# Performance work log

Hardware: AMD Instinct MI355X
Metric: run time of the kernel (lower is better)

The kernel has to match this reference:

```python
import jax, jax.numpy as jnp
import numpy as np

NEG_SLOPE = 0.2  # DGL GATConv default leaky_relu slope

N_NODES, N_EDGES = 50000, 800000
IN_FEATS, HID, OUT_FEATS, HEADS = 256, 64, 64, 3


def gat_conv(x, W, attn_l, attn_r, bias, src, dst, n_nodes, activation=True):
    """DGL-style GATConv. x:[N,F_in], W:[F_in,H*D], attn_l/attn_r/bias:[H,D]."""
    H, D = attn_l.shape
    feat = (x @ W).reshape(n_nodes, H, D)              # [N,H,D]
    el = jnp.sum(feat * attn_l, axis=-1)               # [N,H]
    er = jnp.sum(feat * attn_r, axis=-1)               # [N,H]
    e = jax.nn.leaky_relu(el[src] + er[dst], NEG_SLOPE)  # [E,H]
    # edge softmax over incoming edges of each dst node
    m = jax.ops.segment_max(e, dst, num_segments=n_nodes)  # [N,H] (-inf for isolated)
    ex = jnp.exp(e - m[dst])                            # [E,H]
    s = jax.ops.segment_sum(ex, dst, num_segments=n_nodes)  # [N,H]
    alpha = ex / s[dst]                                 # [E,H]
    msg = feat[src] * alpha[:, :, None]                 # [E,H,D]  (memory-bound gather)
    out = jax.ops.segment_sum(msg, dst, num_segments=n_nodes)  # [N,H,D]
    out = out + bias[None, :, :]
    return jax.nn.relu(out) if activation else out


def setup_inputs() -> dict:
    key = jax.random.key(0)
    ks = jax.random.split(key, 16)
    HD = HEADS * HID
    def glorot(k, shape):
        fan = sum(shape)
        return jax.random.normal(k, shape, jnp.float32) * jnp.sqrt(2.0 / fan)
    return {
        "features": jax.random.normal(ks[0], (N_NODES, IN_FEATS), jnp.float32),
        "src": jax.random.randint(ks[1], (N_EDGES,), 0, N_NODES, jnp.int32),
        "dst": jax.random.randint(ks[2], (N_EDGES,), 0, N_NODES, jnp.int32),
        "W1": glorot(ks[3], (IN_FEATS, HD)),
        "al1": glorot(ks[4], (HEADS, HID)),
        "ar1": glorot(ks[5], (HEADS, HID)),
        "b1": jnp.zeros((HEADS, HID), jnp.float32),
        "W2": glorot(ks[6], (HD, HD)),
        "al2": glorot(ks[7], (HEADS, HID)),
        "ar2": glorot(ks[8], (HEADS, HID)),
        "b2": jnp.zeros((HEADS, HID), jnp.float32),
        "Wm1": glorot(ks[9], (HD, HID)),
        "bm1": jnp.zeros((HID,), jnp.float32),
        "Wm2": glorot(ks[10], (HID, OUT_FEATS)),
        "bm2": jnp.zeros((OUT_FEATS,), jnp.float32),
    }


def reference(features, src, dst, W1, al1, ar1, b1, W2, al2, ar2, b2, Wm1, bm1, Wm2, bm2):
    n = features.shape[0]
    x = gat_conv(features, W1, al1, ar1, b1, src, dst, n).reshape(n, -1)  # [N, H*D]
    x = gat_conv(x, W2, al2, ar2, b2, src, dst, n).reshape(n, -1)        # [N, H*D]
    x = jax.nn.relu(x @ Wm1 + bm1)
    return x @ Wm2 + bm2                                                 # [N, out_feats]
```

## Files before the change

kernel.cpp:

```cpp
#include <hip/hip_runtime.h>
#include <hip/hip_bf16.h>

#define NN 50000
#define NE 800000
#define FIN 256
#define HEADS_H 3
#define HDIM 192
#define NEG_SLOPE 0.2f
#define CHUNK 128
#define SCAN_ELEMS 512
#define SCAN_NB ((NN + SCAN_ELEMS - 1) / SCAN_ELEMS)
#define BK 64
#define W1_PAD 200
#define W2_PAD 72
#define H_PAD 72

typedef __attribute__((ext_vector_type(8))) short frag8;
typedef __attribute__((ext_vector_type(4))) float f32x4;
typedef __attribute__((ext_vector_type(2))) unsigned u32x2;
typedef unsigned short u16;

__device__ inline u16 f2b(float x) {
    __hip_bfloat16 h = __float2bfloat16(x);
    return __builtin_bit_cast(u16, h);
}
__device__ inline float b2f(u16 b) {
    __hip_bfloat16 h = __builtin_bit_cast(__hip_bfloat16, b);
    return __bfloat162float(h);
}
__device__ inline float b2f_lo(unsigned v) { return __builtin_bit_cast(float, v << 16); }
__device__ inline float b2f_hi(unsigned v) { return __builtin_bit_cast(float, v & 0xffff0000u); }

__device__ inline int wave_sum_i(int v) {
#pragma unroll
    for (int off = 32; off > 0; off >>= 1) v += __shfl_xor(v, off, 64);
    return v;
}

__global__ void k_fill_pattern(u16* __restrict__ p, int n, u16 v) {
    int i = blockIdx.x * blockDim.x + threadIdx.x;
    if (i < n) p[i] = v;
}
__global__ void k_zero(int* __restrict__ p, int n) {
    int i = blockIdx.x * blockDim.x + threadIdx.x;
    if (i < n) p[i] = 0;
}

__global__ void k_sniff(const unsigned* __restrict__ p, int* __restrict__ flag) {
    __shared__ int cnt_s;
    if (threadIdx.x == 0) cnt_s = 0;
    __syncthreads();
    int c = 0;
    for (int i = threadIdx.x; i < 4096; i += 256) {
        float v = __builtin_bit_cast(float, p[i]);
        float a = fabsf(v);
        if (a > 1e-4f && a < 100.f) c++;
    }
    atomicAdd(&cnt_s, c);
    __syncthreads();
    if (threadIdx.x == 0) *flag = (cnt_s > 2048) ? 1 : 0;
}

__global__ void k_cvt8(const void* i0, const void* i1, const void* i2, const void* i3,
                       const void* i4, const void* i5, const void* i6, const void* i7,
                       u16* o0, u16* o1, u16* o2, u16* o3, u16* o4, u16* o5, u16* o6, u16* o7,
                       const int* __restrict__ flag) {
    const void* ins[8] = {i0, i1, i2, i3, i4, i5, i6, i7};
    u16* outs[8] = {o0, o1, o2, o3, o4, o5, o6, o7};
    const int ns[8] = {HDIM, HDIM, HDIM, HDIM, HDIM, HDIM, 64, 64};
    int b = blockIdx.x;
    int n = ns[b];
    const void* in = ins[b];
    u16* out = outs[b];
    int f = *flag;
    for (int i = threadIdx.x; i < n; i += 256) {
        out[i] = f ? f2b(((const float*)in)[i]) : ((const u16*)in)[i];
    }
}

__global__ void k_transpose4(const void* __restrict__ B0, const void* __restrict__ B1,
                             const void* __restrict__ B2, const void* __restrict__ B3,
                             u16* __restrict__ T0, u16* __restrict__ T1, u16* __restrict__ T2,
                             u16* __restrict__ T3, const int* __restrict__ flag) {
    const int n0 = FIN * HDIM, n1 = HDIM * HDIM, n2 = HDIM * 64, n3 = 64 * 64;
    int gi = blockIdx.x * 256 + threadIdx.x;
    const void* B;
    u16* T;
    int K, N, i;
    if (gi < n0) { B = B0; T = T0; K = FIN; N = HDIM; i = gi; }
    else if (gi < n0 + n1) { B = B1; T = T1; K = HDIM; N = HDIM; i = gi - n0; }
    else if (gi < n0 + n1 + n2) { B = B2; T = T2; K = HDIM; N = 64; i = gi - n0 - n1; }
    else if (gi < n0 + n1 + n2 + n3) { B = B3; T = T3; K = 64; N = 64; i = gi - n0 - n1 - n2; }
    else return;
    int k = i / N, n = i - k * N;
    u16 v = (*flag) ? f2b(((const float*)B)[i]) : ((const u16*)B)[i];
    T[n * K + k] = v;
}

__global__ void k_count(const int* __restrict__ dst, int* __restrict__ cnt, int E) {
    int e = blockIdx.x * blockDim.x + threadIdx.x;
    if (e < E) atomicAdd(&cnt[dst[e]], 1);
}

__global__ void k_scan_partial(const int* __restrict__ cnt, int* __restrict__ partial) {
    int b = blockIdx.x, t = threadIdx.x;
    int i0 = b * SCAN_ELEMS + t * 2;
    int v = 0;
    if (i0 < NN) v += cnt[i0];
    if (i0 + 1 < NN) v += cnt[i0 + 1];
    v = wave_sum_i(v);
    __shared__ int wsum[4];
    if ((t & 63) == 0) wsum[t >> 6] = v;
    __syncthreads();
    if (t == 0) partial[b] = wsum[0] + wsum[1] + wsum[2] + wsum[3];
}

__global__ void k_scan_mid(const int* __restrict__ partial, int* __restrict__ offsets,
                           int* __restrict__ indptr) {
    __shared__ int s[SCAN_NB];
    int t = threadIdx.x;
    if (t < SCAN_NB) s[t] = partial[t];
    __syncthreads();
    for (int off = 1; off < SCAN_NB; off <<= 1) {
        int v = (t >= off && t < SCAN_NB) ? s[t - off] : 0;
        __syncthreads();
        if (t < SCAN_NB) s[t] += v;
        __syncthreads();
    }
    if (t < SCAN_NB) offsets[t] = (t == 0) ? 0 : s[t - 1];
    if (t == 0) indptr[NN] = s[SCAN_NB - 1];
}

__global__ void k_scan_final(int* __restrict__ cnt, const int* __restrict__ offsets,
                             int* __restrict__ indptr) {
    __shared__ int tsum[256];
    int b = blockIdx.x, t = threadIdx.x;
    int i0 = b * SCAN_ELEMS + t * 2;
    int c0 = (i0 < NN) ? cnt[i0] : 0;
    int c1 = (i0 + 1 < NN) ? cnt[i0 + 1] : 0;
    tsum[t] = c0 + c1;
    __syncthreads();
    for (int off = 1; off < 256; off <<= 1) {
        int v = (t >= off) ? tsum[t - off] : 0;
        __syncthreads();
        tsum[t] += v;
        __syncthreads();
    }
    int excl = offsets[b] + ((t == 0) ? 0 : tsum[t - 1]);
    if (i0 < NN) { indptr[i0] = excl; cnt[i0] = excl; }
    if (i0 + 1 < NN) { indptr[i0 + 1] = excl + c0; cnt[i0 + 1] = excl + c0; }
}

__global__ void k_fill(const int* __restrict__ dst, const int* __restrict__ srcv,
                       int* __restrict__ cursor, int* __restrict__ src_perm, int E) {
    int e = blockIdx.x * blockDim.x + threadIdx.x;
    if (e < E) {
        int p = atomicAdd(&cursor[dst[e]], 1);
        src_perm[p] = srcv[e];
    }
}

__global__ __launch_bounds__(256) void k_gemm_lds(
    const void* __restrict__ A, int a_dual, const u16* __restrict__ BT,
    void* __restrict__ C, const int* __restrict__ flag, int M, int K,
    float* __restrict__ elp, float* __restrict__ erp,
    const u16* __restrict__ al, const u16* __restrict__ ar) {
    __shared__ u16 sB[2][12 * 64 * 8 * 2];
    const int tid = threadIdx.x;
    const int lane = tid & 63;
    const int w = tid >> 6;
    const int c16 = lane & 15;
    const int quad = lane >> 4;
    const int m_base = blockIdx.x * 64 + w * 16;
    const int f = *flag;
    const bool a32 = a_dual && f;

    int m0 = m_base + c16;
    int arow = (m0 < M) ? m0 : (M - 1);

    f32x4 acc[12];
#pragma unroll
    for (int t = 0; t < 12; ++t) acc[t] = (f32x4)0.f;

    frag8 v[6];
    auto stageLoad = [&](int c) {
        int k0 = c * BK;
#pragma unroll
        for (int s = 0; s < 6; ++s) {
            int g = tid + s * 256;
            int n = g >> 3, k8 = g & 7;
            v[s] = *(const frag8*)(BT + (size_t)n * K + k0 + k8 * 8);
        }
    };
    auto stageWrite = [&](int buf) {
#pragma unroll
        for (int s = 0; s < 6; ++s) {
            int g = tid + s * 256;
            int n = g >> 3, k8 = g & 7;
            int t = n >> 4, cc = n & 15, kk = k8 >> 2, qq = k8 & 3;
            int gl = (kk * 12 + t) * 64 + qq * 16 + cc;
            *(frag8*)&sB[buf][gl * 8] = v[s];
        }
    };
    auto loadAc = [&](int k0, frag8* a) {
#pragma unroll
        for (int kk = 0; kk < 2; ++kk) {
            if (a32) {
                const float* ap = (const float*)A + (size_t)arow * K + k0 + kk * 32 + quad * 8;
                f32x4 f0 = *(const f32x4*)ap;
                f32x4 f1 = *(const f32x4*)(ap + 4);
                a[kk][0] = (short)f2b(f0[0]); a[kk][1] = (short)f2b(f0[1]);
                a[kk][2] = (short)f2b(f0[2]); a[kk][3] = (short)f2b(f0[3]);
                a[kk][4] = (short)f2b(f1[0]); a[kk][5] = (short)f2b(f1[1]);
                a[kk][6] = (short)f2b(f1[2]); a[kk][7] = (short)f2b(f1[3]);
            } else {
                a[kk] = *(const frag8*)((const u16*)A + (size_t)arow * K + k0 + kk * 32 + quad * 8);
            }
        }
    };

    const int nc = K / BK;
    stageLoad(0);
    stageWrite(0);
    __syncthreads();
    for (int c = 0; c < nc; ++c) {
        if (c + 1 < nc) stageLoad(c + 1);
        frag8 a[2];
        loadAc(c * BK, a);
        const int buf = c & 1;
#pragma unroll
        for (int kk = 0; kk < 2; ++kk) {
#pragma unroll
            for (int t = 0; t < 12; ++t) {
                frag8 b = *(const frag8*)&sB[buf][((kk * 12 + t) * 64 + lane) * 8];
                acc[t] = __builtin_amdgcn_mfma_f32_16x16x32_bf16(a[kk], b, acc[t], 0, 0, 0);
            }
        }
        if (c + 1 < nc) stageWrite((c + 1) & 1);
        __syncthreads();
    }

#pragma unroll
    for (int t = 0; t < 12; ++t) {
        int col = t * 16 + c16;
#pragma unroll
        for (int rr = 0; rr < 4; ++rr) {
            int m = m_base + quad * 4 + rr;
            if (m < M)
                ((__hip_bfloat16*)C)[(size_t)m * HDIM + col] = __float2bfloat16(acc[t][rr]);
        }
    }

    float alv[12], arv[12];
#pragma unroll
    for (int t = 0; t < 12; ++t) {
        alv[t] = b2f(al[t * 16 + c16]);
        arv[t] = b2f(ar[t * 16 + c16]);
    }
#pragma unroll
    for (int rr = 0; rr < 4; ++rr) {
        int m = m_base + quad * 4 + rr;
        float pl[HEADS_H] = {0.f, 0.f, 0.f};
        float pr[HEADS_H] = {0.f, 0.f, 0.f};
#pragma unroll
        for (int t = 0; t < 12; ++t) {
            int h = t >> 2;
            pl[h] += acc[t][rr] * alv[t];
            pr[h] += acc[t][rr] * arv[t];
        }
#pragma unroll
        for (int h = 0; h < HEADS_H; ++h) {
#pragma unroll
            for (int off = 1; off < 16; off <<= 1) {
                pl[h] += __shfl_xor(pl[h], off, 64);
                pr[h] += __shfl_xor(pr[h], off, 64);
            }
            if (c16 == 0 && m < M) {
                elp[m * HEADS_H + h] = pl[h];
                erp[m * HEADS_H + h] = pr[h];
            }
        }
    }
}

__global__ __launch_bounds__(256) void k_mlp(const u16* __restrict__ xbf,
                                             const u16* __restrict__ Wm1T,
                                             const u16* __restrict__ Wm2T,
                                             const u16* __restrict__ bm1,
                                             const u16* __restrict__ bm2, void* __restrict__ out,
                                             const int* __restrict__ flag, int M) {
    __shared__ u16 sW1[64 * W1_PAD];
    __shared__ u16 sW2[64 * W2_PAD];
    __shared__ u16 sH[64 * H_PAD];
    const int tid = threadIdx.x;
    const int lane = tid & 63, w = tid >> 6;
    const int c16 = lane & 15, quad = lane >> 4;
    const int m_base = blockIdx.x * 64 + w * 16;
    const bool c32 = *flag != 0;

#pragma unroll
    for (int s = 0; s < 6; ++s) {
        int g = tid + s * 256;
        int n = g / 24, k8 = g - n * 24;
        *(frag8*)&sW1[n * W1_PAD + k8 * 8] = *(const frag8*)(Wm1T + n * 192 + k8 * 8);
    }
#pragma unroll
    for (int s = 0; s < 2; ++s) {
        int g = tid + s * 256;
        int n = g >> 3, k8 = g & 7;
        *(frag8*)&sW2[n * W2_PAD + k8 * 8] = *(const frag8*)(Wm2T + n * 64 + k8 * 8);
    }
    int m0 = m_base + c16;
    int arow = (m0 < M) ? m0 : (M - 1);
    __syncthreads();

    f32x4 acc1[4];
#pragma unroll
    for (int t = 0; t < 4; ++t) acc1[t] = (f32x4)0.f;
    for (int k0 = 0; k0 < 192; k0 += 32) {
        frag8 a = *(const frag8*)(xbf + (size_t)arow * HDIM + k0 + quad * 8);
#pragma unroll
        for (int t = 0; t < 4; ++t) {
            frag8 b = *(const frag8*)&sW1[(t * 16 + c16) * W1_PAD + k0 + quad * 8];
            acc1[t] = __builtin_amdgcn_mfma_f32_16x16x32_bf16(a, b, acc1[t], 0, 0, 0);
        }
    }
#pragma unroll
    for (int t = 0; t < 4; ++t) {
        float bv = b2f(bm1[t * 16 + c16]);
#pragma unroll
        for (int rr = 0; rr < 4; ++rr) {
            float v = fmaxf(acc1[t][rr] + bv, 0.f);
            sH[(w * 16 + quad * 4 + rr) * H_PAD + t * 16 + c16] = f2b(v);
        }
    }
    __syncthreads();

    f32x4 acc2[4];
#pragma unroll
    for (int t = 0; t < 4; ++t) acc2[t] = (f32x4)0.f;
#pragma unroll
    for (int k0 = 0; k0 < 64; k0 += 32) {
        frag8 a = *(const frag8*)&sH[(w * 16 + c16) * H_PAD + k0 + quad * 8];
#pragma unroll
        for (int t = 0; t < 4; ++t) {
            frag8 b = *(const frag8*)&sW2[(t * 16 + c16) * W2_PAD + k0 + quad * 8];
            acc2[t] = __builtin_amdgcn_mfma_f32_16x16x32_bf16(a, b, acc2[t], 0, 0, 0);
        }
    }
#pragma unroll
    for (int t = 0; t < 4; ++t) {
        int col = t * 16 + c16;
        float bv = b2f(bm2[col]);
#pragma unroll
        for (int rr = 0; rr < 4; ++rr) {
            int m = m_base + quad * 4 + rr;
            if (m < M) {
                float v = acc2[t][rr] + bv;
                if (c32) ((float*)out)[(size_t)m * 64 + col] = v;
                else ((__hip_bfloat16*)out)[(size_t)m * 64 + col] = __float2bfloat16(v);
            }
        }
    }
}

__global__ __launch_bounds__(256) void k_agg_sm(
    const u16* __restrict__ feat, const float* __restrict__ el, const float* __restrict__ er,
    const int* __restrict__ src_perm, const int* __restrict__ indptr,
    const u16* __restrict__ bias, u16* __restrict__ outb, int n_nodes) {
    __shared__ int ssrc_s[4][CHUNK];
    __shared__ float salpha_s[4][CHUNK * HEADS_H];
    const int wave = threadIdx.x >> 6, lane = threadIdx.x & 63;
    const int n = blockIdx.x * 4 + wave;
    if (n >= n_nodes) return;
    int* ssrc = ssrc_s[wave];
    float* salpha = salpha_s[wave];
    const int beg = indptr[n];
    const int lenT = indptr[n + 1] - beg;
    const float er0 = er[n * 3 + 0], er1 = er[n * 3 + 1], er2 = er[n * 3 + 2];
    const int u = lane;
    const int h = u >> 4;
    const u16* fbase = feat + 4 * u;

    float m0 = -INFINITY, m1 = -INFINITY, m2 = -INFINITY;
    float s0 = 0.f, s1 = 0.f, s2 = 0.f;
    float a0 = 0.f, a1 = 0.f, a2 = 0.f, a3 = 0.f;

    for (int c0 = 0; c0 < lenT; c0 += CHUNK) {
        const int len = min(CHUNK, lenT - c0);
        float cm0 = -INFINITY, cm1 = -INFINITY, cm2 = -INFINITY;
        for (int j = lane; j < len; j += 64) {
            int s = src_perm[beg + c0 + j];
            ssrc[j] = s;
            const float* ep = el + (size_t)s * 3;
            float e0 = ep[0] + er0, e1 = ep[1] + er1, e2 = ep[2] + er2;
            e0 = (e0 > 0.f) ? e0 : NEG_SLOPE * e0;
            e1 = (e1 > 0.f) ? e1 : NEG_SLOPE * e1;
            e2 = (e2 > 0.f) ? e2 : NEG_SLOPE * e2;
            salpha[j * 3 + 0] = e0;
            salpha[j * 3 + 1] = e1;
            salpha[j * 3 + 2] = e2;
            cm0 = fmaxf(cm0, e0); cm1 = fmaxf(cm1, e1); cm2 = fmaxf(cm2, e2);
        }
#pragma unroll
        for (int off = 32; off > 0; off >>= 1) {
            cm0 = fmaxf(cm0, __shfl_xor(cm0, off, 64));
            cm1 = fmaxf(cm1, __shfl_xor(cm1, off, 64));
            cm2 = fmaxf(cm2, __shfl_xor(cm2, off, 64));
        }
        float n0 = fmaxf(m0, cm0), n1 = fmaxf(m1, cm1), n2 = fmaxf(m2, cm2);
        float r0 = __expf(m0 - n0), r1 = __expf(m1 - n1), r2 = __expf(m2 - n2);
        __threadfence_block();
        float cs0 = 0.f, cs1 = 0.f, cs2 = 0.f;
        for (int j = lane; j < len; j += 64) {
            float ex0 = __expf(salpha[j * 3 + 0] - n0);
            float ex1 = __expf(salpha[j * 3 + 1] - n1);
            float ex2 = __expf(salpha[j * 3 + 2] - n2);
            salpha[j * 3 + 0] = ex0;
            salpha[j * 3 + 1] = ex1;
            salpha[j * 3 + 2] = ex2;
            cs0 += ex0; cs1 += ex1; cs2 += ex2;
        }
#pragma unroll
        for (int off = 32; off > 0; off >>= 1) {
            cs0 += __shfl_xor(cs0, off, 64);
            cs1 += __shfl_xor(cs1, off, 64);
            cs2 += __shfl_xor(cs2, off, 64);
        }
        s0 = s0 * r0 + cs0; s1 = s1 * r1 + cs1; s2 = s2 * r2 + cs2;
        m0 = n0; m1 = n1; m2 = n2;
        __threadfence_block();
        if (u < 48) {
            float rh = (h == 0) ? r0 : ((h == 1) ? r1 : r2);
            a0 *= rh; a1 *= rh; a2 *= rh; a3 *= rh;
            for (int j0 = 0; j0 < len; j0 += 4) {
                int jb = min(j0 + 1, len - 1), jc = min(j0 + 2, len - 1), jd = min(j0 + 3, len - 1);
                int sa = ssrc[j0], sb = ssrc[jb], sc = ssrc[jc], sd = ssrc[jd];
                float wa = salpha[j0 * 3 + h];
                float wb = (j0 + 1 < len) ? salpha[jb * 3 + h] : 0.f;
                float wc = (j0 + 2 < len) ? salpha[jc * 3 + h] : 0.f;
                float wd = (j0 + 3 < len) ? salpha[jd * 3 + h] : 0.f;
                u32x2 va = *(const u32x2*)(fbase + (size_t)sa * HDIM);
                u32x2 vb = *(const u32x2*)(fbase + (size_t)sb * HDIM);
                u32x2 vc = *(const u32x2*)(fbase + (size_t)sc * HDIM);
                u32x2 vd = *(const u32x2*)(fbase + (size_t)sd * HDIM);
                a0 += wa * b2f_lo(va.x); a1 += wa * b2f_hi(va.x);
                a2 += wa * b2f_lo(va.y); a3 += wa * b2f_hi(va.y);
                a0 += wb * b2f_lo(vb.x); a1 += wb * b2f_hi(vb.x);
                a2 += wb * b2f_lo(vb.y); a3 += wb * b2f_hi(vb.y);
                a0 += wc * b2f_lo(vc.x); a1 += wc * b2f_hi(vc.x);
                a2 += wc * b2f_lo(vc.y); a3 += wc * b2f_hi(vc.y);
                a0 += wd * b2f_lo(vd.x); a1 += wd * b2f_hi(vd.x);
                a2 += wd * b2f_lo(vd.y); a3 += wd * b2f_hi(vd.y);
            }
        }
    }

    if (u < 48) {
        float shh = (h == 0) ? s0 : ((h == 1) ? s1 : s2);
        float inv = (shh > 0.f) ? 1.f / shh : 0.f;
        u32x2 bv = *(const u32x2*)(bias + 4 * u);
        float v0 = a0 * inv + b2f_lo(bv.x);
        float v1 = a1 * inv + b2f_hi(bv.x);
        float v2 = a2 * inv + b2f_lo(bv.y);
        float v3 = a3 * inv + b2f_hi(bv.y);
        v0 = fmaxf(v0, 0.f); v1 = fmaxf(v1, 0.f);
        v2 = fmaxf(v2, 0.f); v3 = fmaxf(v3, 0.f);
        u32x2 o;
        o.x = (unsigned)f2b(v0) | ((unsigned)f2b(v1) << 16);
        o.y = (unsigned)f2b(v2) | ((unsigned)f2b(v3) << 16);
        *(u32x2*)(outb + (size_t)n * HDIM + 4 * u) = o;
    }
}

extern "C" void kernel_launch(void* const* d_in, const int* in_sizes, int n_in,
                              void* d_out, int out_size, void* d_ws, size_t ws_size,
                              hipStream_t stream) {
    const void* features = d_in[0];
    const int* src = (const int*)d_in[1];
    const int* dst = (const int*)d_in[2];
    const void* W1 = d_in[3];
    const void* al1 = d_in[4];
    const void* ar1 = d_in[5];
    const void* b1 = d_in[6];
    const void* W2 = d_in[7];
    const void* al2 = d_in[8];
    const void* ar2 = d_in[9];
    const void* b2 = d_in[10];
    const void* Wm1 = d_in[11];
    const void* bm1 = d_in[12];
    const void* Wm2 = d_in[13];
    const void* bm2 = d_in[14];

    char* ws = (char*)d_ws;
    size_t off = 0;
    auto alloc = [&](size_t bytes) -> void* {
        void* p = ws + off;
        off = (off + bytes + 255) & ~(size_t)255;
        return p;
    };
    int* flag = (int*)alloc(4);
    u16* featb = (u16*)alloc((size_t)NN * HDIM * 2);
    u16* xbf = (u16*)alloc((size_t)NN * HDIM * 2);
    float* el = (float*)alloc((size_t)NN * HEADS_H * 4);
    float* er = (float*)alloc((size_t)NN * HEADS_H * 4);
    int* indptr = (int*)alloc((size_t)(NN + 1) * 4);
    int* cnt = (int*)alloc((size_t)NN * 4);
    int* src_perm = (int*)alloc((size_t)NE * 4);
    int* partial = (int*)alloc((size_t)SCAN_NB * 4);
    int* offsets = (int*)alloc((size_t)SCAN_NB * 4);
    u16* W1T = (u16*)alloc((size_t)FIN * HDIM * 2);
    u16* W2T = (u16*)alloc((size_t)HDIM * HDIM * 2);
    u16* Wm1T = (u16*)alloc((size_t)HDIM * 64 * 2);
    u16* Wm2T = (u16*)alloc((size_t)64 * 64 * 2);
    u16* al1c = (u16*)alloc(HDIM * 2);
    u16* ar1c = (u16*)alloc(HDIM * 2);
    u16* b1c = (u16*)alloc(HDIM * 2);
    u16* al2c = (u16*)alloc(HDIM * 2);
    u16* ar2c = (u16*)alloc(HDIM * 2);
    u16* b2c = (u16*)alloc(HDIM * 2);
    u16* bm1c = (u16*)alloc(64 * 2);
    u16* bm2c = (u16*)alloc(64 * 2);

    if (ws_size < off) {
        k_fill_pattern<<<(out_size + 255) / 256, 256, 0, stream>>>((u16*)d_out, out_size, 0x3F80);
        return;
    }

    k_sniff<<<1, 256, 0, stream>>>((const unsigned*)features, flag);

    k_cvt8<<<8, 256, 0, stream>>>(al1, ar1, b1, al2, ar2, b2, bm1, bm2, al1c, ar1c, b1c, al2c,
                                  ar2c, b2c, bm1c, bm2c, flag);
    {
        const int tot = FIN * HDIM + HDIM * HDIM + HDIM * 64 + 64 * 64;
        k_transpose4<<<(tot + 255) / 256, 256, 0, stream>>>(W1, W2, Wm1, Wm2, W1T, W2T, Wm1T,
                                                            Wm2T, flag);
    }

    k_zero<<<(NN + 255) / 256, 256, 0, stream>>>(cnt, NN);
    k_count<<<(NE + 255) / 256, 256, 0, stream>>>(dst, cnt, NE);
    k_scan_partial<<<SCAN_NB, 256, 0, stream>>>(cnt, partial);
    k_scan_mid<<<1, 128, 0, stream>>>(partial, offsets, indptr);
    k_scan_final<<<SCAN_NB, 256, 0, stream>>>(cnt, offsets, indptr);
    k_fill<<<(NE + 255) / 256, 256, 0, stream>>>(dst, src, cnt, src_perm, NE);

    const int g64 = (NN + 63) / 64;
    const int gagg = (NN + 3) / 4;

    k_gemm_lds<<<g64, 256, 0, stream>>>(features, 1, W1T, featb, flag, NN, FIN, el, er, al1c,
                                        ar1c);
    k_agg_sm<<<gagg, 256, 0, stream>>>(featb, el, er, src_perm, indptr, b1c, xbf, NN);

    k_gemm_lds<<<g64, 256, 0, stream>>>(xbf, 0, W2T, featb, flag, NN, HDIM, el, er, al2c, ar2c);
    k_agg_sm<<<gagg, 256, 0, stream>>>(featb, el, er, src_perm, indptr, b2c, xbf, NN);

    k_mlp<<<g64, 256, 0, stream>>>(xbf, Wm1T, Wm2T, bm1c, bm2c, d_out, flag, NN);
}
```

Before: 373.1 us.

## Build CSR via two-level bucket sort with LDS histograms

```diff
diff --git a/kernel.cpp b/kernel.cpp
--- a/kernel.cpp
+++ b/kernel.cpp
@@ -8,12 +8,12 @@
 #define HDIM 192
 #define NEG_SLOPE 0.2f
 #define CHUNK 128
-#define SCAN_ELEMS 512
-#define SCAN_NB ((NN + SCAN_ELEMS - 1) / SCAN_ELEMS)
 #define BK 64
 #define W1_PAD 200
 #define W2_PAD 72
 #define H_PAD 72
+#define BSH 6
+#define NBUCK ((NN + 63) >> BSH)
 
 typedef __attribute__((ext_vector_type(8))) short frag8;
 typedef __attribute__((ext_vector_type(4))) float f32x4;
@@ -30,12 +30,6 @@
 }
 __device__ inline float b2f_lo(unsigned v) { return __builtin_bit_cast(float, v << 16); }
 __device__ inline float b2f_hi(unsigned v) { return __builtin_bit_cast(float, v & 0xffff0000u); }
-
-__device__ inline int wave_sum_i(int v) {
-#pragma unroll
-    for (int off = 32; off > 0; off >>= 1) v += __shfl_xor(v, off, 64);
-    return v;
-}
 
 __global__ void k_fill_pattern(u16* __restrict__ p, int n, u16 v) {
     int i = blockIdx.x * blockDim.x + threadIdx.x;
@@ -97,66 +91,85 @@
     T[n * K + k] = v;
 }
 
-__global__ void k_count(const int* __restrict__ dst, int* __restrict__ cnt, int E) {
-    int e = blockIdx.x * blockDim.x + threadIdx.x;
-    if (e < E) atomicAdd(&cnt[dst[e]], 1);
-}
-
-__global__ void k_scan_partial(const int* __restrict__ cnt, int* __restrict__ partial) {
-    int b = blockIdx.x, t = threadIdx.x;
-    int i0 = b * SCAN_ELEMS + t * 2;
-    int v = 0;
-    if (i0 < NN) v += cnt[i0];
-    if (i0 + 1 < NN) v += cnt[i0 + 1];
-    v = wave_sum_i(v);
-    __shared__ int wsum[4];
-    if ((t & 63) == 0) wsum[t >> 6] = v;
-    __syncthreads();
-    if (t == 0) partial[b] = wsum[0] + wsum[1] + wsum[2] + wsum[3];
-}
-
-__global__ void k_scan_mid(const int* __restrict__ partial, int* __restrict__ offsets,
-                           int* __restrict__ indptr) {
-    __shared__ int s[SCAN_NB];
+__global__ __launch_bounds__(256) void k_bhist(const int* __restrict__ dst,
+                                               int* __restrict__ bhist) {
+    __shared__ int lh[NBUCK];
+    for (int i = threadIdx.x; i < NBUCK; i += 256) lh[i] = 0;
+    __syncthreads();
+    const int per = (NE + gridDim.x - 1) / gridDim.x;
+    int e0 = blockIdx.x * per, e1 = min(e0 + per, NE);
+    for (int e = e0 + threadIdx.x; e < e1; e += 256) atomicAdd(&lh[dst[e] >> BSH], 1);
+    __syncthreads();
+    for (int i = threadIdx.x; i < NBUCK; i += 256) {
+        int v = lh[i];
+        if (v) atomicAdd(&bhist[i], v);
+    }
+}
+
+__global__ __launch_bounds__(1024) void k_bscan(const int* __restrict__ bhist,
+                                                int* __restrict__ boffset,
+                                                int* __restrict__ bcursor) {
+    __shared__ int s[1024];
     int t = threadIdx.x;
-    if (t < SCAN_NB) s[t] = partial[t];
-    __syncthreads();
-    for (int off = 1; off < SCAN_NB; off <<= 1) {
-        int v = (t >= off && t < SCAN_NB) ? s[t - off] : 0;
+    s[t] = (t < NBUCK) ? bhist[t] : 0;
+    __syncthreads();
+    for (int off = 1; off < 1024; off <<= 1) {
+        int v = (t >= off) ? s[t - off] : 0;
         __syncthreads();
-        if (t < SCAN_NB) s[t] += v;
+        s[t] += v;
         __syncthreads();
     }
-    if (t < SCAN_NB) offsets[t] = (t == 0) ? 0 : s[t - 1];
-    if (t == 0) indptr[NN] = s[SCAN_NB - 1];
-}
-
-__global__ void k_scan_final(int* __restrict__ cnt, const int* __restrict__ offsets,
-                             int* __restrict__ indptr) {
-    __shared__ int tsum[256];
-    int b = blockIdx.x, t = threadIdx.x;
-    int i0 = b * SCAN_ELEMS + t * 2;
-    int c0 = (i0 < NN) ? cnt[i0] : 0;
-    int c1 = (i0 + 1 < NN) ? cnt[i0 + 1] : 0;
-    tsum[t] = c0 + c1;
-    __syncthreads();
-    for (int off = 1; off < 256; off <<= 1) {
-        int v = (t >= off) ? tsum[t - off] : 0;
-        __syncthreads();
-        tsum[t] += v;
-        __syncthreads();
-    }
-    int excl = offsets[b] + ((t == 0) ? 0 : tsum[t - 1]);
-    if (i0 < NN) { indptr[i0] = excl; cnt[i0] = excl; }
-    if (i0 + 1 < NN) { indptr[i0 + 1] = excl + c0; cnt[i0 + 1] = excl + c0; }
-}
-
-__global__ void k_fill(const int* __restrict__ dst, const int* __restrict__ srcv,
-                       int* __restrict__ cursor, int* __restrict__ src_perm, int E) {
+    if (t < NBUCK) {
+        int excl = (t == 0) ? 0 : s[t - 1];
+        boffset[t] = excl;
+        bcursor[t] = excl;
+    }
+    if (t == 0) boffset[NBUCK] = NE;
+}
+
+__global__ void k_bscatter(const int* __restrict__ dst, const int* __restrict__ srcv,
+                           int* __restrict__ bcursor, u32x2* __restrict__ bpairs, int E) {
     int e = blockIdx.x * blockDim.x + threadIdx.x;
     if (e < E) {
-        int p = atomicAdd(&cursor[dst[e]], 1);
-        src_perm[p] = srcv[e];
+        int d = dst[e];
+        int p = atomicAdd(&bcursor[d >> BSH], 1);
+        u32x2 pr;
+        pr.x = (unsigned)srcv[e];
+        pr.y = (unsigned)d;
+        bpairs[p] = pr;
+    }
+}
+
+__global__ __launch_bounds__(256) void k_bucket_csr(const u32x2* __restrict__ bpairs,
+                                                    const int* __restrict__ boffset,
+                                                    int* __restrict__ indptr,
+                                                    int* __restrict__ src_perm) {
+    __shared__ int cnt[64];
+    __shared__ int cur[64];
+    const int b = blockIdx.x, t = threadIdx.x;
+    const int pbeg = boffset[b], pend = boffset[b + 1];
+    if (t < 64) cnt[t] = 0;
+    __syncthreads();
+    for (int i = pbeg + t; i < pend; i += 256) atomicAdd(&cnt[bpairs[i].y & 63], 1);
+    __syncthreads();
+    if (t < 64) {
+        int v = cnt[t];
+        int iv = v;
+        for (int off = 1; off < 64; off <<= 1) {
+            int u = __shfl_up(iv, off, 64);
+            if (t >= off) iv += u;
+        }
+        int excl = iv - v;
+        cur[t] = excl;
+        int node = (b << BSH) + t;
+        if (node < NN) indptr[node] = pbeg + excl;
+        if (b == NBUCK - 1 && t == 63) indptr[NN] = NE;
+    }
+    __syncthreads();
+    for (int i = pbeg + t; i < pend; i += 256) {
+        u32x2 pr = bpairs[i];
+        int p = atomicAdd(&cur[pr.y & 63], 1);
+        src_perm[pbeg + p] = (int)pr.x;
     }
 }
 
@@ -505,10 +518,11 @@
     float* el = (float*)alloc((size_t)NN * HEADS_H * 4);
     float* er = (float*)alloc((size_t)NN * HEADS_H * 4);
     int* indptr = (int*)alloc((size_t)(NN + 1) * 4);
-    int* cnt = (int*)alloc((size_t)NN * 4);
     int* src_perm = (int*)alloc((size_t)NE * 4);
-    int* partial = (int*)alloc((size_t)SCAN_NB * 4);
-    int* offsets = (int*)alloc((size_t)SCAN_NB * 4);
+    u32x2* bpairs = (u32x2*)alloc((size_t)NE * 8);
+    int* bhist = (int*)alloc((size_t)NBUCK * 4);
+    int* boffset = (int*)alloc((size_t)(NBUCK + 1) * 4);
+    int* bcursor = (int*)alloc((size_t)NBUCK * 4);
     u16* W1T = (u16*)alloc((size_t)FIN * HDIM * 2);
     u16* W2T = (u16*)alloc((size_t)HDIM * HDIM * 2);
     u16* Wm1T = (u16*)alloc((size_t)HDIM * 64 * 2);
@@ -537,12 +551,11 @@
                                                             Wm2T, flag);
     }
 
-    k_zero<<<(NN + 255) / 256, 256, 0, stream>>>(cnt, NN);
-    k_count<<<(NE + 255) / 256, 256, 0, stream>>>(dst, cnt, NE);
-    k_scan_partial<<<SCAN_NB, 256, 0, stream>>>(cnt, partial);
-    k_scan_mid<<<1, 128, 0, stream>>>(partial, offsets, indptr);
-    k_scan_final<<<SCAN_NB, 256, 0, stream>>>(cnt, offsets, indptr);
-    k_fill<<<(NE + 255) / 256, 256, 0, stream>>>(dst, src, cnt, src_perm, NE);
+    k_zero<<<(NBUCK + 255) / 256, 256, 0, stream>>>(bhist, NBUCK);
+    k_bhist<<<256, 256, 0, stream>>>(dst, bhist);
+    k_bscan<<<1, 1024, 0, stream>>>(bhist, boffset, bcursor);
+    k_bscatter<<<(NE + 255) / 256, 256, 0, stream>>>(dst, src, bcursor, bpairs, NE);
+    k_bucket_csr<<<NBUCK, 256, 0, stream>>>(bpairs, boffset, indptr, src_perm);
 
     const int g64 = (NN + 63) / 64;
     const int gagg = (NN + 3) / 4;
```

After: 493.1 us. 1.32x slower.
